# Optimization experiments

Measured on AMD Instinct MI355X. Metric: run time of the kernel, lower is better.

Reference implementation:

```python
import jax, jax.numpy as jnp
import numpy as np

EPS = 1e-5
NEG_SLOPE = 0.01

def layer_norm(x, w, b):
    m = jnp.mean(x, axis=-1, keepdims=True)
    v = jnp.var(x, axis=-1, keepdims=True)
    return (x - m) / jnp.sqrt(v + EPS) * w + b

def _lin_init(key, out_dim, in_dim):
    s = 1.0 / np.sqrt(in_dim)
    k1, k2 = jax.random.split(key)
    W = jax.random.uniform(k1, (out_dim, in_dim), jnp.float32, -s, s)
    b = jax.random.uniform(k2, (out_dim,), jnp.float32, -s, s)
    return W, b

def setup_inputs() -> dict:
    key = jax.random.key(0)
    ks = jax.random.split(key, 12)
    N_S = 100000; N_T = 100000; E = 2000000; H1 = 64; H2 = 32
    x_s = jax.random.normal(ks[0], (N_S, 2), jnp.float32)
    x_t = jax.random.normal(ks[1], (N_T, 2), jnp.float32)
    edge_index = jax.random.randint(ks[2], (2, E), 0, N_S, jnp.int32)
    edge_attr = jax.random.uniform(ks[3], (E,), jnp.float32)
    w0, b0 = _lin_init(ks[4], H1, 3)
    w1, b1 = _lin_init(ks[5], H1, H1)
    w2, b2 = _lin_init(ks[6], H1, H1)
    w3, b3 = _lin_init(ks[7], 1, H1)
    ln_w = jnp.ones((3, H1), jnp.float32)
    ln_b = jnp.zeros((3, H1), jnp.float32)
    fw1, fb1 = _lin_init(ks[8], H2, 4)
    fln_w = jnp.ones((H2,), jnp.float32)
    fln_b = jnp.zeros((H2,), jnp.float32)
    fw2, fb2 = _lin_init(ks[9], 1, H2)
    return dict(x_s=x_s, x_t=x_t, edge_index=edge_index, edge_attr=edge_attr,
                w0=w0, b0=b0, w1=w1, b1=b1, w2=w2, b2=b2, w3=w3, b3=b3,
                ln_w=ln_w, ln_b=ln_b, fw1=fw1, fb1=fb1, fln_w=fln_w, fln_b=fln_b,
                fw2=fw2, fb2=fb2)

def reference(x_s, x_t, edge_index, edge_attr, w0, b0, w1, b1, w2, b2, w3, b3,
              ln_w, ln_b, fw1, fb1, fln_w, fln_b, fw2, fb2):
    src = edge_index[0]
    dst = edge_index[1]
    x_s_d = x_s[src, 1][:, None]           # [E,1]
    x_s_c = x_t[dst, 1][:, None]           # [E,1]
    y = jnp.concatenate([x_s_d, x_s_c, edge_attr[:, None]], axis=1)  # [E,3]
    # MLP chain: Linear -> LeakyReLU -> (dropout eval: identity) -> LayerNorm
    for i, (W, b) in enumerate([(w0, b0), (w1, b1), (w2, b2)]):
        y = layer_norm(jax.nn.leaky_relu(y @ W.T + b, NEG_SLOPE), ln_w[i], ln_b[i])
    y = jax.nn.relu(y @ w3.T + b3)[:, 0]   # [E]
    # index_add scatter then re-gather
    y_sum_i = jax.ops.segment_sum(y, src, num_segments=x_s.shape[0])[src][:, None]
    y_sum_j = jax.ops.segment_sum(y, dst, num_segments=x_t.shape[0])[dst][:, None]
    coef = jnp.concatenate([x_s_d, y_sum_i, x_s_c, y_sum_j], axis=1)  # [E,4]
    coef = layer_norm(jax.nn.relu(coef @ fw1.T + fb1), fln_w, fln_b)
    coef = jax.nn.relu(coef @ fw2.T + fb2)[:, 0]
    return y * coef
```

## Files before the change

kernel.cpp:

```cpp
#include <hip/hip_runtime.h>

#define H2 32

#define SIG_F32  0x3F800000u
#define SIG_BF16 0x3F803F80u

typedef float v4f __attribute__((ext_vector_type(4)));
typedef short s8v __attribute__((ext_vector_type(8)));
typedef unsigned u4v __attribute__((ext_vector_type(4)));

__global__ void zero_f(float* __restrict__ p, int n) {
    int i = blockIdx.x * blockDim.x + threadIdx.x;
    if (i < n) p[i] = 0.0f;
}

template<bool BF16>
__device__ __forceinline__ float LD(const void* p, int i) {
    if (BF16) {
        unsigned int u = ((unsigned int)((const unsigned short*)p)[i]) << 16;
        return __uint_as_float(u);
    }
    return ((const float*)p)[i];
}

template<bool BF16>
__device__ __forceinline__ void ST(void* p, int i, float v) {
    if (BF16) {
        unsigned int u = __float_as_uint(v);
        unsigned int r = (u + 0x7FFFu + ((u >> 16) & 1u)) >> 16;
        ((unsigned short*)p)[i] = (unsigned short)r;
    } else {
        ((float*)p)[i] = v;
    }
}

__device__ __forceinline__ unsigned short bf16_rne(float x) {
    unsigned int u = __float_as_uint(x);
    return (unsigned short)((u + 0x7FFFu + ((u >> 16) & 1u)) >> 16);
}

__device__ __forceinline__ void split2(float x0, float x1,
                                       unsigned& hw, unsigned& lw) {
    unsigned h;
    asm("v_cvt_pk_bf16_f32 %0, %1, %2" : "=v"(h) : "v"(x0), "v"(x1));
    const float h0 = __uint_as_float(h << 16);
    const float h1 = __uint_as_float(h & 0xFFFF0000u);
    unsigned l;
    asm("v_cvt_pk_bf16_f32 %0, %1, %2" : "=v"(l) : "v"(x0 - h0), "v"(x1 - h1));
    hw = h; lw = l;
}

__device__ __align__(16) unsigned short g_A[2 * 2 * 4 * 2 * 512];
__device__ __align__(16) float g_S[2][64], g_C[2][64];
__device__ __align__(16) float g_l0[64 * 4];
__device__ __align__(16) float g_w3g[64];
__device__ float g_sc3[2];

template<bool BF16>
__global__ void setup_fold_t(const void* __restrict__ w0, const void* __restrict__ b0,
                             const void* __restrict__ w1, const void* __restrict__ b1,
                             const void* __restrict__ w2, const void* __restrict__ b2,
                             const void* __restrict__ w3, const void* __restrict__ b3,
                             const void* __restrict__ lnw, const void* __restrict__ lnb) {
    const unsigned int sig = *(const unsigned int*)lnw;
    if (sig != (BF16 ? SIG_BF16 : SIG_F32)) return;
    const int b = blockIdx.x;
    const int k = threadIdx.x;
    if (b < 128) {
        const int L = b >> 6, j = b & 63;
        const void* w  = L ? w2 : w1;
        const void* bb = L ? b2 : b1;
        const float wv = LD<BF16>(w, j * 64 + k);
        const float wt = wv * LD<BF16>(lnw, L * 64 + k);
        float s = wt;
        float c = wv * LD<BF16>(lnb, L * 64 + k);
        #pragma unroll
        for (int off = 1; off < 64; off <<= 1) {
            s += __shfl_xor(s, off);
            c += __shfl_xor(c, off);
        }
        if (k == 0) {
            g_S[L][j] = s;
            g_C[L][j] = c + LD<BF16>(bb, j);
        }
    } else {
        const int j = k;
        g_l0[4 * j + 0] = LD<BF16>(w0, 3 * j);
        g_l0[4 * j + 1] = LD<BF16>(w0, 3 * j + 1);
        g_l0[4 * j + 2] = LD<BF16>(w0, 3 * j + 2);
        g_l0[4 * j + 3] = LD<BF16>(b0, j);
        const float w3g = LD<BF16>(w3, j) * LD<BF16>(lnw, 128 + j);
        g_w3g[j] = w3g;
        float S = w3g;
        float C = LD<BF16>(w3, j) * LD<BF16>(lnb, 128 + j);
        #pragma unroll
        for (int off = 1; off < 64; off <<= 1) {
            S += __shfl_xor(S, off);
            C += __shfl_xor(C, off);
        }
        if (j == 0) { g_sc3[0] = S; g_sc3[1] = C + LD<BF16>(b3, 0); }
    }
}

template<bool BF16>
__global__ void setup_frag_t(const void* __restrict__ w1, const void* __restrict__ w2,
                             const void* __restrict__ lnw) {
    const unsigned int sig = *(const unsigned int*)lnw;
    if (sig != (BF16 ? SIG_BF16 : SIG_F32)) return;
    const int b  = blockIdx.x;
    const int L  = b >> 3, jt = (b >> 1) & 3, ks = b & 1;
    const int l  = threadIdx.x, m = l & 15, g = l >> 4;
    const void* w = L ? w2 : w1;
    const int row = 16 * jt + m;
    const int blkH = ((L * 2 + 0) * 4 + jt) * 2 + ks;
    const int blkL = ((L * 2 + 1) * 4 + jt) * 2 + ks;
    #pragma unroll
    for (int i = 0; i < 8; ++i) {
        const int k = 32 * ks + 8 * g + i;
        const float x = LD<BF16>(w, row * 64 + k) * LD<BF16>(lnw, L * 64 + k);
        const unsigned short hi = bf16_rne(x);
        const float hif = __uint_as_float(((unsigned int)hi) << 16);
        const unsigned short lo = bf16_rne(x - hif);
        g_A[blkH * 512 + l * 8 + i] = hi;
        g_A[blkL * 512 + l * 8 + i] = lo;
    }
}

template<bool BF16>
__global__ __launch_bounds__(256, 2)
void edge_mfma_t(const void* __restrict__ xs, const void* __restrict__ xt,
                 const int* __restrict__ ei, const void* __restrict__ ea,
                 const void* __restrict__ lnw,
                 void* __restrict__ ystage,
                 float* __restrict__ ssrc, float* __restrict__ sdst, int E) {
    const unsigned int sig = *(const unsigned int*)lnw;
    if (sig != (BF16 ? SIG_BF16 : SIG_F32)) return;

    __shared__ __align__(16) unsigned char lds[4][8192];
    const int tid = threadIdx.x;
    const int l   = tid & 63;
    const int wid = __builtin_amdgcn_readfirstlane(tid >> 6);
    unsigned char* Hb = &lds[wid][0];
    const int m16 = l & 15, g = l >> 4;

    const int tile = blockIdx.x * 4 + wid;
    const int e0 = tile * 32;
    if (e0 >= E) return;

    int srcA[2], dstA[2];
    float av[2], cv[2], wv[2];
    #pragma unroll
    for (int s = 0; s < 2; ++s) {
        int e = e0 + s * 16 + m16;
        int ec = e < E ? e : 0;
        srcA[s] = ei[ec]; dstA[s] = ei[E + ec];
        av[s] = LD<BF16>(xs, 2 * srcA[s] + 1);
        cv[s] = LD<BF16>(xt, 2 * dstA[s] + 1);
        wv[s] = LD<BF16>(ea, ec);
    }

    float m_[2], r_[2];

    s8v Bh[2][2], Bl[2][2];
    {
        float ps[2] = {0.f, 0.f}, ps2[2] = {0.f, 0.f};
        #pragma unroll
        for (int s = 0; s < 2; ++s) {
            #pragma unroll
            for (int ks = 0; ks < 2; ++ks) {
                u4v th, tl;
                #pragma unroll
                for (int q = 0; q < 4; ++q) {
                    const int f = 32 * ks + 8 * g + 2 * q;
                    const v4f qa = *(const v4f*)&g_l0[4 * f];
                    const v4f qb = *(const v4f*)&g_l0[4 * (f + 1)];
                    float x0 = qa.w + av[s] * qa.x + cv[s] * qa.y + wv[s] * qa.z;
                    float x1 = qb.w + av[s] * qb.x + cv[s] * qb.y + wv[s] * qb.z;
                    x0 = fmaxf(x0, 0.01f * x0);
                    x1 = fmaxf(x1, 0.01f * x1);
                    ps[s] += x0 + x1; ps2[s] += x0 * x0 + x1 * x1;
                    unsigned hw, lw;
                    split2(x0, x1, hw, lw);
                    th[q] = hw; tl[q] = lw;
                }
                Bh[s][ks] = __builtin_bit_cast(s8v, th);
                Bl[s][ks] = __builtin_bit_cast(s8v, tl);
            }
            float a0 = ps[s], a1 = ps2[s];
            a0 += __shfl_xor(a0, 16); a0 += __shfl_xor(a0, 32);
            a1 += __shfl_xor(a1, 16); a1 += __shfl_xor(a1, 32);
            m_[s] = a0 * (1.f / 64.f);
            r_[s] = rsqrtf(a1 * (1.f / 64.f) - m_[s] * m_[s] + 1e-5f);
        }
    }

    {
        float psA[2] = {0.f, 0.f}, ps2A[2] = {0.f, 0.f};
        #pragma unroll
        for (int jt = 0; jt < 4; ++jt) {
            const s8v Ah0 = *(const s8v*)(g_A + ((0 + jt) * 2 + 0) * 512 + l * 8);
            const s8v Ah1 = *(const s8v*)(g_A + ((0 + jt) * 2 + 1) * 512 + l * 8);
            const s8v Al0 = *(const s8v*)(g_A + ((4 + jt) * 2 + 0) * 512 + l * 8);
            const s8v Al1 = *(const s8v*)(g_A + ((4 + jt) * 2 + 1) * 512 + l * 8);
            const v4f Sv = *(const v4f*)&g_S[0][16 * jt + 4 * g];
            const v4f Cv = *(const v4f*)&g_C[0][16 * jt + 4 * g];
            #pragma unroll
            for (int s = 0; s < 2; ++s) {
                v4f a0 = {0.f, 0.f, 0.f, 0.f};
                v4f a1 = {0.f, 0.f, 0.f, 0.f};
                a0 = __builtin_amdgcn_mfma_f32_16x16x32_bf16(Ah0, Bh[s][0], a0, 0, 0, 0);
                a1 = __builtin_amdgcn_mfma_f32_16x16x32_bf16(Al0, Bh[s][0], a1, 0, 0, 0);
                a0 = __builtin_amdgcn_mfma_f32_16x16x32_bf16(Ah1, Bh[s][1], a0, 0, 0, 0);
                a1 = __builtin_amdgcn_mfma_f32_16x16x32_bf16(Al1, Bh[s][1], a1, 0, 0, 0);
                a0 = __builtin_amdgcn_mfma_f32_16x16x32_bf16(Ah0, Bl[s][0], a0, 0, 0, 0);
                a1 = __builtin_amdgcn_mfma_f32_16x16x32_bf16(Ah1, Bl[s][1], a1, 0, 0, 0);
                float x0 = r_[s] * ((a0[0] + a1[0]) - m_[s] * Sv[0]) + Cv[0];
                float x1 = r_[s] * ((a0[1] + a1[1]) - m_[s] * Sv[1]) + Cv[1];
                float x2 = r_[s] * ((a0[2] + a1[2]) - m_[s] * Sv[2]) + Cv[2];
                float x3 = r_[s] * ((a0[3] + a1[3]) - m_[s] * Sv[3]) + Cv[3];
                x0 = fmaxf(x0, 0.01f * x0); x1 = fmaxf(x1, 0.01f * x1);
                x2 = fmaxf(x2, 0.01f * x2); x3 = fmaxf(x3, 0.01f * x3);
                psA[s]  += x0 + x1 + x2 + x3;
                ps2A[s] += x0 * x0 + x1 * x1 + x2 * x2 + x3 * x3;
                unsigned hw0, lw0, hw1, lw1;
                split2(x0, x1, hw0, lw0);
                split2(x2, x3, hw1, lw1);
                const int el = s * 16 + m16;
                const unsigned sw = (unsigned)((el & 7) << 4);
                const unsigned off = (unsigned)el * 128
                                   + (((unsigned)(32 * jt + 8 * g)) ^ sw);
                uint2 ph; ph.x = hw0; ph.y = hw1;
                uint2 pl; pl.x = lw0; pl.y = lw1;
                *(uint2*)&Hb[off] = ph;
                *(uint2*)&Hb[off + 4096] = pl;
            }
        }
        #pragma unroll
        for (int s = 0; s < 2; ++s) {
            float ps = psA[s], ps2 = ps2A[s];
            ps  += __shfl_xor(ps, 16);  ps  += __shfl_xor(ps, 32);
            ps2 += __shfl_xor(ps2, 16); ps2 += __shfl_xor(ps2, 32);
            m_[s] = ps * (1.f / 64.f);
            r_[s] = rsqrtf(ps2 * (1.f / 64.f) - m_[s] * m_[s] + 1e-5f);
        }
    }

    float pd[2] = {0.f, 0.f};
    {
        #pragma unroll
        for (int s = 0; s < 2; ++s) {
            const int el = s * 16 + m16;
            const unsigned sw = (unsigned)((el & 7) << 4);
            #pragma unroll
            for (int ks = 0; ks < 2; ++ks) {
                const unsigned off = (unsigned)el * 128
                                   + (((unsigned)(16 * g + 64 * ks)) ^ sw);
                Bh[s][ks] = *(const s8v*)&Hb[off];
                Bl[s][ks] = *(const s8v*)&Hb[off + 4096];
            }
        }
        float psA[2] = {0.f, 0.f}, ps2A[2] = {0.f, 0.f};
        #pragma unroll
        for (int jt = 0; jt < 4; ++jt) {
            const s8v Ah0 = *(const s8v*)(g_A + ((8  + jt) * 2 + 0) * 512 + l * 8);
            const s8v Ah1 = *(const s8v*)(g_A + ((8  + jt) * 2 + 1) * 512 + l * 8);
            const s8v Al0 = *(const s8v*)(g_A + ((12 + jt) * 2 + 0) * 512 + l * 8);
            const s8v Al1 = *(const s8v*)(g_A + ((12 + jt) * 2 + 1) * 512 + l * 8);
            const v4f Sv = *(const v4f*)&g_S[1][16 * jt + 4 * g];
            const v4f Cv = *(const v4f*)&g_C[1][16 * jt + 4 * g];
            const v4f w3v = *(const v4f*)&g_w3g[16 * jt + 4 * g];
            #pragma unroll
            for (int s = 0; s < 2; ++s) {
                v4f a0 = {0.f, 0.f, 0.f, 0.f};
                v4f a1 = {0.f, 0.f, 0.f, 0.f};
                a0 = __builtin_amdgcn_mfma_f32_16x16x32_bf16(Ah0, Bh[s][0], a0, 0, 0, 0);
                a1 = __builtin_amdgcn_mfma_f32_16x16x32_bf16(Al0, Bh[s][0], a1, 0, 0, 0);
                a0 = __builtin_amdgcn_mfma_f32_16x16x32_bf16(Ah1, Bh[s][1], a0, 0, 0, 0);
                a1 = __builtin_amdgcn_mfma_f32_16x16x32_bf16(Al1, Bh[s][1], a1, 0, 0, 0);
                a0 = __builtin_amdgcn_mfma_f32_16x16x32_bf16(Ah0, Bl[s][0], a0, 0, 0, 0);
                a1 = __builtin_amdgcn_mfma_f32_16x16x32_bf16(Ah1, Bl[s][1], a1, 0, 0, 0);
                #pragma unroll
                for (int r = 0; r < 4; ++r) {
                    float x = r_[s] * ((a0[r] + a1[r]) - m_[s] * Sv[r]) + Cv[r];
                    x = fmaxf(x, 0.01f * x);
                    psA[s] += x; ps2A[s] += x * x;
                    pd[s] += x * w3v[r];
                }
            }
        }
        #pragma unroll
        for (int s = 0; s < 2; ++s) {
            float ps = psA[s], ps2 = ps2A[s];
            ps  += __shfl_xor(ps, 16);  ps  += __shfl_xor(ps, 32);
            ps2 += __shfl_xor(ps2, 16); ps2 += __shfl_xor(ps2, 32);
            m_[s] = ps * (1.f / 64.f);
            r_[s] = rsqrtf(ps2 * (1.f / 64.f) - m_[s] * m_[s] + 1e-5f);
        }
    }

    #pragma unroll
    for (int s = 0; s < 2; ++s) {
        float d = pd[s];
        d += __shfl_xor(d, 16); d += __shfl_xor(d, 32);
        float t = r_[s] * (d - m_[s] * g_sc3[0]) + g_sc3[1];
        const float yv = fmaxf(t, 0.f);
        if (g == 0) {
            int e = e0 + s * 16 + m16;
            if (e < E) {
                ST<BF16>(ystage, e, yv);
                atomicAdd(&ssrc[srcA[s]], yv);
                atomicAdd(&sdst[dstA[s]], yv);
            }
        }
    }
}

template<bool BF16>
__global__ __launch_bounds__(256)
void coef_stage_t(const void* __restrict__ xs, const void* __restrict__ xt,
                  const int* __restrict__ ei,
                  const void* __restrict__ fw1, const void* __restrict__ fb1,
                  const void* __restrict__ flnw, const void* __restrict__ flnb,
                  const void* __restrict__ fw2, const void* __restrict__ fb2,
                  const void* __restrict__ lnw,
                  const float* __restrict__ ssrc, const float* __restrict__ sdst,
                  void* __restrict__ out, int E) {
    const unsigned int sig = *(const unsigned int*)lnw;
    if (sig != (BF16 ? SIG_BF16 : SIG_F32)) return;
    int e = blockIdx.x * blockDim.x + threadIdx.x;
    if (e >= E) return;
    const int src = ei[e], dst = ei[E + e];
    const float c0 = LD<BF16>(xs, 2 * src + 1);
    const float c2 = LD<BF16>(xt, 2 * dst + 1);
    const float c1 = ssrc[src];
    const float c3 = sdst[dst];
    float h[H2];
    float sum = 0.f, sum2 = 0.f;
    #pragma unroll
    for (int j = 0; j < H2; ++j) {
        float t = LD<BF16>(fb1, j) + c0 * LD<BF16>(fw1, 4 * j) + c1 * LD<BF16>(fw1, 4 * j + 1)
                + c2 * LD<BF16>(fw1, 4 * j + 2) + c3 * LD<BF16>(fw1, 4 * j + 3);
        t = (t > 0.f) ? t : 0.f;
        h[j] = t; sum += t; sum2 += t * t;
    }
    const float m = sum * (1.f / H2);
    const float r = rsqrtf(sum2 * (1.f / H2) - m * m + 1e-5f);
    float t = LD<BF16>(fb2, 0);
    #pragma unroll
    for (int j = 0; j < H2; ++j)
        t += ((h[j] - m) * r * LD<BF16>(flnw, j) + LD<BF16>(flnb, j)) * LD<BF16>(fw2, j);
    const float coef = (t > 0.f) ? t : 0.f;
    const float yv = LD<BF16>(out, e);
    ST<BF16>(out, e, yv * coef);
}

extern "C" void kernel_launch(void* const* d_in, const int* in_sizes, int n_in,
                              void* d_out, int out_size, void* d_ws, size_t ws_size,
                              hipStream_t stream) {
    const void* xs = d_in[0];
    const void* xt = d_in[1];
    const int*  ei = (const int*)d_in[2];
    const void* ea = d_in[3];
    const int NS = in_sizes[0] / 2;
    const int NT = in_sizes[1] / 2;
    const int E  = in_sizes[3];

    float* ws   = (float*)d_ws;
    float* ssrc = ws;
    float* sdst = ws + NS;

    const int nz = NS + NT;
    const int gE = (E + 255) / 256;
    zero_f<<<(nz + 255) / 256, 256, 0, stream>>>(ws, nz);

    setup_fold_t<false><<<129, 64, 0, stream>>>(
        d_in[4], d_in[5], d_in[6], d_in[7], d_in[8], d_in[9],
        d_in[10], d_in[11], d_in[12], d_in[13]);
    setup_fold_t<true><<<129, 64, 0, stream>>>(
        d_in[4], d_in[5], d_in[6], d_in[7], d_in[8], d_in[9],
        d_in[10], d_in[11], d_in[12], d_in[13]);
    setup_frag_t<false><<<16, 64, 0, stream>>>(d_in[6], d_in[8], d_in[12]);
    setup_frag_t<true><<<16, 64, 0, stream>>>(d_in[6], d_in[8], d_in[12]);

    const int tiles  = (E + 31) / 32;
    const int blocks = (tiles + 3) / 4;
    edge_mfma_t<false><<<blocks, 256, 0, stream>>>(
        xs, xt, ei, ea, d_in[12], d_out, ssrc, sdst, E);
    edge_mfma_t<true><<<blocks, 256, 0, stream>>>(
        xs, xt, ei, ea, d_in[12], d_out, ssrc, sdst, E);

    coef_stage_t<false><<<gE, 256, 0, stream>>>(
        xs, xt, ei, d_in[14], d_in[15], d_in[16], d_in[17], d_in[18], d_in[19],
        d_in[12], ssrc, sdst, d_out, E);
    coef_stage_t<true><<<gE, 256, 0, stream>>>(
        xs, xt, ei, d_in[14], d_in[15], d_in[16], d_in[17], d_in[18], d_in[19],
        d_in[12], ssrc, sdst, d_out, E);
}
```

Baseline: 372.4 us.

## Process two edge tiles per wave with gathers for both issued upfront

The edge MLP kernel now handles two 32-edge tiles per wave instead of one. It issues the index and feature gathers for both tiles before computing either, so the second tile's random-access loads overlap with the first tile's MFMA work. This halves the grid size and raises register pressure, which may hurt occupancy under the 256x2 launch bound.

```diff
diff --git a/kernel.cpp b/kernel.cpp
--- a/kernel.cpp
+++ b/kernel.cpp
@@ -126,38 +126,17 @@
     }
 }
 
-template<bool BF16>
-__global__ __launch_bounds__(256, 2)
-void edge_mfma_t(const void* __restrict__ xs, const void* __restrict__ xt,
-                 const int* __restrict__ ei, const void* __restrict__ ea,
-                 const void* __restrict__ lnw,
-                 void* __restrict__ ystage,
-                 float* __restrict__ ssrc, float* __restrict__ sdst, int E) {
-    const unsigned int sig = *(const unsigned int*)lnw;
-    if (sig != (BF16 ? SIG_BF16 : SIG_F32)) return;
-
-    __shared__ __align__(16) unsigned char lds[4][8192];
-    const int tid = threadIdx.x;
-    const int l   = tid & 63;
-    const int wid = __builtin_amdgcn_readfirstlane(tid >> 6);
-    unsigned char* Hb = &lds[wid][0];
-    const int m16 = l & 15, g = l >> 4;
-
-    const int tile = blockIdx.x * 4 + wid;
-    const int e0 = tile * 32;
-    if (e0 >= E) return;
-
-    int srcA[2], dstA[2];
+struct EdgeData {
+    int   src[2], dst[2];
     float av[2], cv[2], wv[2];
-    #pragma unroll
-    for (int s = 0; s < 2; ++s) {
-        int e = e0 + s * 16 + m16;
-        int ec = e < E ? e : 0;
-        srcA[s] = ei[ec]; dstA[s] = ei[E + ec];
-        av[s] = LD<BF16>(xs, 2 * srcA[s] + 1);
-        cv[s] = LD<BF16>(xt, 2 * dstA[s] + 1);
-        wv[s] = LD<BF16>(ea, ec);
-    }
+};
+
+template<bool BF16>
+__device__ __forceinline__ void tile_body(
+    int e0, const EdgeData& ed,
+    unsigned char* Hb, int m16, int g, int l, int E,
+    void* __restrict__ ystage, float* __restrict__ ssrc,
+    float* __restrict__ sdst) {
 
     float m_[2], r_[2];
 
@@ -174,8 +153,8 @@
                     const int f = 32 * ks + 8 * g + 2 * q;
                     const v4f qa = *(const v4f*)&g_l0[4 * f];
                     const v4f qb = *(const v4f*)&g_l0[4 * (f + 1)];
-                    float x0 = qa.w + av[s] * qa.x + cv[s] * qa.y + wv[s] * qa.z;
-                    float x1 = qb.w + av[s] * qb.x + cv[s] * qb.y + wv[s] * qb.z;
+                    float x0 = qa.w + ed.av[s] * qa.x + ed.cv[s] * qa.y + ed.wv[s] * qa.z;
+                    float x1 = qb.w + ed.av[s] * qb.x + ed.cv[s] * qb.y + ed.wv[s] * qb.z;
                     x0 = fmaxf(x0, 0.01f * x0);
                     x1 = fmaxf(x1, 0.01f * x1);
                     ps[s] += x0 + x1; ps2[s] += x0 * x0 + x1 * x1;
@@ -308,11 +287,62 @@
             int e = e0 + s * 16 + m16;
             if (e < E) {
                 ST<BF16>(ystage, e, yv);
-                atomicAdd(&ssrc[srcA[s]], yv);
-                atomicAdd(&sdst[dstA[s]], yv);
+                atomicAdd(&ssrc[ed.src[s]], yv);
+                atomicAdd(&sdst[ed.dst[s]], yv);
             }
         }
     }
+}
+
+template<bool BF16>
+__global__ __launch_bounds__(256, 2)
+void edge_mfma_t(const void* __restrict__ xs, const void* __restrict__ xt,
+                 const int* __restrict__ ei, const void* __restrict__ ea,
+                 const void* __restrict__ lnw,
+                 void* __restrict__ ystage,
+                 float* __restrict__ ssrc, float* __restrict__ sdst, int E) {
+    const unsigned int sig = *(const unsigned int*)lnw;
+    if (sig != (BF16 ? SIG_BF16 : SIG_F32)) return;
+
+    __shared__ __align__(16) unsigned char lds[4][8192];
+    const int tid = threadIdx.x;
+    const int l   = tid & 63;
+    const int wid = __builtin_amdgcn_readfirstlane(tid >> 6);
+    unsigned char* Hb = &lds[wid][0];
+    const int m16 = l & 15, g = l >> 4;
+
+    const int pair = blockIdx.x * 4 + wid;
+    const int e0A = pair * 64;
+    if (e0A >= E) return;
+    const int e0B = e0A + 32;
+
+    EdgeData edA, edB;
+    #pragma unroll
+    for (int s = 0; s < 2; ++s) {
+        int e = e0A + s * 16 + m16;
+        int ec = e < E ? e : 0;
+        edA.src[s] = ei[ec]; edA.dst[s] = ei[E + ec];
+        edA.av[s] = LD<BF16>(xs, 2 * edA.src[s] + 1);
+        edA.cv[s] = LD<BF16>(xt, 2 * edA.dst[s] + 1);
+        edA.wv[s] = LD<BF16>(ea, ec);
+    }
+    #pragma unroll
+    for (int s = 0; s < 2; ++s) {
+        int e = e0B + s * 16 + m16;
+        int ec = e < E ? e : 0;
+        edB.src[s] = ei[ec]; edB.dst[s] = ei[E + ec];
+        edB.av[s] = LD<BF16>(xs, 2 * edB.src[s] + 1);
+        edB.cv[s] = LD<BF16>(xt, 2 * edB.dst[s] + 1);
+        edB.wv[s] = LD<BF16>(ea, ec);
+    }
+
+    tile_body<BF16>(e0A, edA, Hb, m16, g, l, E, ystage, ssrc, sdst);
+
+    asm volatile("" ::: "memory");
+    __builtin_amdgcn_sched_barrier(0);
+
+    if (e0B < E)
+        tile_body<BF16>(e0B, edB, Hb, m16, g, l, E, ystage, ssrc, sdst);
 }
 
 template<bool BF16>
@@ -382,8 +412,8 @@
     setup_frag_t<false><<<16, 64, 0, stream>>>(d_in[6], d_in[8], d_in[12]);
     setup_frag_t<true><<<16, 64, 0, stream>>>(d_in[6], d_in[8], d_in[12]);
 
-    const int tiles  = (E + 31) / 32;
-    const int blocks = (tiles + 3) / 4;
+    const int pairs  = (E + 63) / 64;
+    const int blocks = (pairs + 3) / 4;
     edge_mfma_t<false><<<blocks, 256, 0, stream>>>(
         xs, xt, ei, ea, d_in[12], d_out, ssrc, sdst, E);
     edge_mfma_t<true><<<blocks, 256, 0, stream>>>(
```

New measurement: 398.5 us. 7.0% more time.
